# Performance work log

Measured on AMD Instinct MI355X. Metric: run time of the kernel, lower is better.

## Reference

```python
import jax, jax.numpy as jnp
import numpy as np

N, E, FEAT, C, H, D, L, T, MS, MD, NC = 20000, 320000, 128, 256, 8, 32, 5, 64, 10, 128, 2
NEG_SLOPE = 0.2


def setup_inputs() -> dict:
    key = jax.random.key(0)
    ks = jax.random.split(key, 20)
    g = lambda k, shape, fan: jax.random.normal(k, shape, jnp.float32) / np.sqrt(fan)
    return {
        "x_initial_nodes": jax.random.normal(ks[0], (N, FEAT), jnp.float32),
        "edge_index": jax.random.randint(ks[1], (2, E), 0, N, jnp.int32),
        "time_embedding": jax.random.normal(ks[2], (N, T), jnp.float32),
        "Wi": g(ks[3], (FEAT, C), FEAT),
        "bi": jnp.zeros((C,), jnp.float32),
        "Wg": g(ks[4], (L, C, C), C),          # GAT projection per layer
        "a_src": g(ks[5], (L, H, D), D),        # attention vectors
        "a_dst": g(ks[6], (L, H, D), D),
        "Wt": g(ks[7], (L, T, C), T),           # time-embedding fusion
        "Wq": g(ks[8], (L, C, C), C),           # memory cross-attention
        "Wk": g(ks[9], (L, MD, C), MD),
        "Wv": g(ks[10], (L, MD, C), MD),
        "global_memory": jax.random.normal(ks[11], (MS, MD), jnp.float32),
        "Wc": g(ks[12], (C + MD, NC), C + MD),
        "bc": jnp.zeros((NC,), jnp.float32),
    }


def _stm_layer(x, src, dst, t_proj, mem, Wg, a_s, a_d, Wq, Wk, Wv):
    # GAT-style message passing with time fusion
    h = ((x + t_proj) @ Wg).reshape(N, H, D)                      # [N,H,D]
    e_src = jnp.einsum('nhd,hd->nh', h, a_s)                      # [N,H]
    e_dst = jnp.einsum('nhd,hd->nh', h, a_d)
    logits = jax.nn.leaky_relu(e_src[src] + e_dst[dst], NEG_SLOPE)  # [E,H]
    m = jax.ops.segment_max(logits, dst, num_segments=N)
    m = jnp.where(jnp.isfinite(m), m, 0.0)                        # empty segments
    ex = jnp.exp(logits - m[dst])
    denom = jax.ops.segment_sum(ex, dst, num_segments=N)
    alpha = ex / (denom[dst] + 1e-16)                             # [E,H]
    msg = jax.ops.segment_sum(alpha[:, :, None] * h[src], dst, num_segments=N)
    node = jax.nn.relu(msg.reshape(N, C))
    # cross-attention to global memory bank
    q = node @ Wq                                                  # [N,C]
    k = mem @ Wk                                                   # [MS,C]
    v = mem @ Wv                                                   # [MS,C]
    attn = jax.nn.softmax(q @ k.T / np.sqrt(C), axis=-1)           # [N,MS]
    return jax.nn.relu(node + attn @ v + x)                        # residual


def reference(x_initial_nodes, edge_index, time_embedding, Wi, bi, Wg, a_src,
              a_dst, Wt, Wq, Wk, Wv, global_memory, Wc, bc):
    src, dst = edge_index[0], edge_index[1]
    node = jax.nn.relu(x_initial_nodes @ Wi + bi)                  # [N,C]
    for l in range(L):
        t_proj = time_embedding @ Wt[l]                            # [N,C]
        node = _stm_layer(node, src, dst, t_proj, global_memory,
                          Wg[l], a_src[l], a_dst[l], Wq[l], Wk[l], Wv[l])
    pooled = jnp.mean(node, axis=0)                                # [C]
    mem_pooled = jnp.mean(global_memory, axis=0)                   # [MD]
    final = jnp.concatenate([pooled, mem_pooled], axis=-1)         # [C+MD]
    return final @ Wc + bc                                         # [NC]
```

## Files before the change

### kernel.cpp

```cpp
#include <hip/hip_runtime.h>
#include <hip/hip_bf16.h>

#define N_NODES 20000
#define E_EDGES 320000
#define FEAT 128
#define CDIM 256
#define NHEAD 8
#define HDIM 32
#define NLAYER 5
#define TDIM 64
#define MSLOT 10
#define MDIM 128
#define NCLS 2

typedef unsigned short ushort_t;
typedef short short8 __attribute__((ext_vector_type(8)));
typedef float floatx4 __attribute__((ext_vector_type(4)));

__device__ __forceinline__ ushort_t f2bf(float f) {
    union { float f; unsigned int u; } t; t.f = f;
    unsigned int r = (t.u + 0x7FFF + ((t.u >> 16) & 1)) >> 16;
    return (ushort_t)r;
}
__device__ __forceinline__ float bf2f(ushort_t u) {
    union { float f; unsigned int u; } t; t.u = ((unsigned int)u) << 16;
    return t.f;
}

__global__ __launch_bounds__(256) void gemm_mfma(
    const ushort_t* __restrict__ A1, int lda1, int K1,
    const ushort_t* __restrict__ A2, int lda2, int Ktot,
    const ushort_t* __restrict__ Bt,
    const float* __restrict__ bias,
    float* Cf, ushort_t* Cbf, int doRelu, int M)
{
    __shared__ __align__(16) ushort_t smemA[64 * 32];
    __shared__ __align__(16) ushort_t smemB[256 * 32];
    int tid = threadIdx.x;
    int lane = tid & 63, wid = tid >> 6;
    int li = lane & 15, lq = lane >> 4;
    int row0 = blockIdx.x * 64;

    floatx4 acc[4][4];
#pragma unroll
    for (int a = 0; a < 4; a++)
#pragma unroll
        for (int b = 0; b < 4; b++) acc[a][b] = {0.f, 0.f, 0.f, 0.f};

    int ar = tid >> 2, ac = tid & 3;
    int agc = (ac - (ar >> 1)) & 3;
    int arow = row0 + ar; if (arow >= M) arow = M - 1;

    for (int k0 = 0; k0 < Ktot; k0 += 32) {
        __syncthreads();
        const ushort_t* Ab; int lda;
        if (k0 < K1) { Ab = A1 + k0; lda = lda1; }
        else         { Ab = A2 + (k0 - K1); lda = lda2; }
        {
            const void* g = (const void*)(Ab + (size_t)arow * lda + agc * 8);
            __builtin_amdgcn_global_load_lds(
                (const __attribute__((address_space(1))) void*)g,
                (__attribute__((address_space(3))) void*)&smemA[wid * 512], 16, 0, 0);
        }
#pragma unroll
        for (int j = 0; j < 4; j++) {
            int slot = wid * 256 + j * 64 + lane;
            int n = slot >> 2, c = slot & 3;
            int gc = (c - (n >> 1)) & 3;
            const void* g = (const void*)(Bt + (size_t)n * Ktot + k0 + gc * 8);
            __builtin_amdgcn_global_load_lds(
                (const __attribute__((address_space(1))) void*)g,
                (__attribute__((address_space(3))) void*)&smemB[(wid * 256 + j * 64) * 8], 16, 0, 0);
        }
        __syncthreads();

        short8 af[4], bfr[4];
#pragma unroll
        for (int mt = 0; mt < 4; mt++) {
            int m = mt * 16 + li;
            int sw = (lq + (m >> 1)) & 3;
            af[mt] = *(const short8*)&smemA[m * 32 + sw * 8];
        }
#pragma unroll
        for (int nt = 0; nt < 4; nt++) {
            int n = wid * 64 + nt * 16 + li;
            int sw = (lq + (n >> 1)) & 3;
            bfr[nt] = *(const short8*)&smemB[n * 32 + sw * 8];
        }
#pragma unroll
        for (int mt = 0; mt < 4; mt++)
#pragma unroll
            for (int nt = 0; nt < 4; nt++)
                acc[mt][nt] = __builtin_amdgcn_mfma_f32_16x16x32_bf16(af[mt], bfr[nt], acc[mt][nt], 0, 0, 0);
    }

#pragma unroll
    for (int mt = 0; mt < 4; mt++) {
        int row = row0 + mt * 16 + lq * 4;
#pragma unroll
        for (int nt = 0; nt < 4; nt++) {
            int col = wid * 64 + nt * 16 + li;
            float bv = bias ? bias[col] : 0.f;
#pragma unroll
            for (int r = 0; r < 4; r++) {
                if (row + r < M) {
                    float v = acc[mt][nt][r] + bv;
                    if (doRelu) v = fmaxf(v, 0.f);
                    if (Cf)  Cf[(size_t)(row + r) * CDIM + col] = v;
                    if (Cbf) Cbf[(size_t)(row + r) * CDIM + col] = f2bf(v);
                }
            }
        }
    }
}

__global__ __launch_bounds__(256) void gemm_h(
    const ushort_t* __restrict__ A1, int lda1, int K1,
    const ushort_t* __restrict__ A2, int lda2, int Ktot,
    const ushort_t* __restrict__ Bt,
    const float* __restrict__ a_s, const float* __restrict__ a_d,
    ushort_t* __restrict__ Cbf,
    float* __restrict__ esrc, float* __restrict__ edst, int M)
{
    __shared__ __align__(16) ushort_t smemA[64 * 32];
    __shared__ __align__(16) ushort_t smemB[256 * 32];
    __shared__ float eldsS[64][8];
    __shared__ float eldsD[64][8];
    int tid = threadIdx.x;
    int lane = tid & 63, wid = tid >> 6;
    int li = lane & 15, lq = lane >> 4;
    int row0 = blockIdx.x * 64;

    floatx4 acc[4][4];
#pragma unroll
    for (int a = 0; a < 4; a++)
#pragma unroll
        for (int b = 0; b < 4; b++) acc[a][b] = {0.f, 0.f, 0.f, 0.f};

    int ar = tid >> 2, ac = tid & 3;
    int agc = (ac - (ar >> 1)) & 3;
    int arow = row0 + ar; if (arow >= M) arow = M - 1;

    for (int k0 = 0; k0 < Ktot; k0 += 32) {
        __syncthreads();
        const ushort_t* Ab; int lda;
        if (k0 < K1) { Ab = A1 + k0; lda = lda1; }
        else         { Ab = A2 + (k0 - K1); lda = lda2; }
        {
            const void* g = (const void*)(Ab + (size_t)arow * lda + agc * 8);
            __builtin_amdgcn_global_load_lds(
                (const __attribute__((address_space(1))) void*)g,
                (__attribute__((address_space(3))) void*)&smemA[wid * 512], 16, 0, 0);
        }
#pragma unroll
        for (int j = 0; j < 4; j++) {
            int slot = wid * 256 + j * 64 + lane;
            int n = slot >> 2, c = slot & 3;
            int gc = (c - (n >> 1)) & 3;
            const void* g = (const void*)(Bt + (size_t)n * Ktot + k0 + gc * 8);
            __builtin_amdgcn_global_load_lds(
                (const __attribute__((address_space(1))) void*)g,
                (__attribute__((address_space(3))) void*)&smemB[(wid * 256 + j * 64) * 8], 16, 0, 0);
        }
        __syncthreads();

        short8 af[4], bfr[4];
#pragma unroll
        for (int mt = 0; mt < 4; mt++) {
            int m = mt * 16 + li;
            int sw = (lq + (m >> 1)) & 3;
            af[mt] = *(const short8*)&smemA[m * 32 + sw * 8];
        }
#pragma unroll
        for (int nt = 0; nt < 4; nt++) {
            int n = wid * 64 + nt * 16 + li;
            int sw = (lq + (n >> 1)) & 3;
            bfr[nt] = *(const short8*)&smemB[n * 32 + sw * 8];
        }
#pragma unroll
        for (int mt = 0; mt < 4; mt++)
#pragma unroll
            for (int nt = 0; nt < 4; nt++)
                acc[mt][nt] = __builtin_amdgcn_mfma_f32_16x16x32_bf16(af[mt], bfr[nt], acc[mt][nt], 0, 0, 0);
    }

    float as4[4], ad4[4];
#pragma unroll
    for (int nt = 0; nt < 4; nt++) {
        int col = wid * 64 + nt * 16 + li;
        as4[nt] = a_s[col];
        ad4[nt] = a_d[col];
    }
#pragma unroll
    for (int mt = 0; mt < 4; mt++) {
        int row = row0 + mt * 16 + lq * 4;
#pragma unroll
        for (int nt = 0; nt < 4; nt++) {
            int col = wid * 64 + nt * 16 + li;
#pragma unroll
            for (int r = 0; r < 4; r++)
                if (row + r < M)
                    Cbf[(size_t)(row + r) * CDIM + col] = f2bf(acc[mt][nt][r]);
        }
#pragma unroll
        for (int r = 0; r < 4; r++) {
            int row_local = mt * 16 + lq * 4 + r;
            float psA = acc[mt][0][r] * as4[0] + acc[mt][1][r] * as4[1];
            float psB = acc[mt][2][r] * as4[2] + acc[mt][3][r] * as4[3];
            float pdA = acc[mt][0][r] * ad4[0] + acc[mt][1][r] * ad4[1];
            float pdB = acc[mt][2][r] * ad4[2] + acc[mt][3][r] * ad4[3];
#pragma unroll
            for (int d = 1; d < 16; d <<= 1) {
                psA += __shfl_xor(psA, d); psB += __shfl_xor(psB, d);
                pdA += __shfl_xor(pdA, d); pdB += __shfl_xor(pdB, d);
            }
            if (li == 0) {
                eldsS[row_local][2 * wid + 0] = psA;
                eldsS[row_local][2 * wid + 1] = psB;
                eldsD[row_local][2 * wid + 0] = pdA;
                eldsD[row_local][2 * wid + 1] = pdB;
            }
        }
    }
    __syncthreads();
#pragma unroll
    for (int rr = 0; rr < 2; rr++) {
        int row = rr * 32 + (tid >> 3), hh = tid & 7;
        if (row0 + row < M) {
            esrc[(size_t)(row0 + row) * NHEAD + hh] = eldsS[row][hh];
            edst[(size_t)(row0 + row) * NHEAD + hh] = eldsD[row][hh];
        }
    }
}

__global__ __launch_bounds__(256) void gemm64(
    const float* __restrict__ A, const float* __restrict__ A2,
    const float* __restrict__ B, const float* __restrict__ bias,
    float* __restrict__ C, int M, int K, int Nf, int doRelu,
    int sA, int sB, int sC)
{
    __shared__ float As[16][64];
    __shared__ float Bs[16][64];
    A += (size_t)blockIdx.z * sA;
    B += (size_t)blockIdx.z * sB;
    C += (size_t)blockIdx.z * sC;
    int tid = threadIdx.x;
    int tx = tid & 15, ty = tid >> 4;
    int row0 = blockIdx.y * 64, col0 = blockIdx.x * 64;
    int ar = tid >> 2;
    int ac = (tid & 3) * 4;

    float acc[4][4] = {};

    for (int k0 = 0; k0 < K; k0 += 16) {
        int arow = row0 + ar;
        float4 av = make_float4(0.f, 0.f, 0.f, 0.f);
        if (arow < M) {
            av = *(const float4*)(A + (size_t)arow * K + k0 + ac);
            if (A2) {
                float4 a2 = *(const float4*)(A2 + (size_t)arow * K + k0 + ac);
                av.x += a2.x; av.y += a2.y; av.z += a2.z; av.w += a2.w;
            }
        }
        As[ac + 0][ar] = av.x;
        As[ac + 1][ar] = av.y;
        As[ac + 2][ar] = av.z;
        As[ac + 3][ar] = av.w;
        float4 bv = *(const float4*)(B + (size_t)(k0 + (tid >> 4)) * Nf + col0 + (tid & 15) * 4);
        *(float4*)&Bs[tid >> 4][(tid & 15) * 4] = bv;
        __syncthreads();
#pragma unroll
        for (int kk = 0; kk < 16; kk++) {
            float4 a = *(const float4*)&As[kk][ty * 4];
            float4 b = *(const float4*)&Bs[kk][tx * 4];
            acc[0][0] += a.x * b.x; acc[0][1] += a.x * b.y; acc[0][2] += a.x * b.z; acc[0][3] += a.x * b.w;
            acc[1][0] += a.y * b.x; acc[1][1] += a.y * b.y; acc[1][2] += a.y * b.z; acc[1][3] += a.y * b.w;
            acc[2][0] += a.z * b.x; acc[2][1] += a.z * b.y; acc[2][2] += a.z * b.z; acc[2][3] += a.z * b.w;
            acc[3][0] += a.w * b.x; acc[3][1] += a.w * b.y; acc[3][2] += a.w * b.z; acc[3][3] += a.w * b.w;
        }
        __syncthreads();
    }

    float4 bv = make_float4(0.f, 0.f, 0.f, 0.f);
    if (bias) bv = *(const float4*)(bias + col0 + tx * 4);
#pragma unroll
    for (int i = 0; i < 4; i++) {
        int r = row0 + ty * 4 + i;
        if (r < M) {
            float4 o;
            o.x = acc[i][0] + bv.x;
            o.y = acc[i][1] + bv.y;
            o.z = acc[i][2] + bv.z;
            o.w = acc[i][3] + bv.w;
            if (doRelu) {
                o.x = fmaxf(o.x, 0.f); o.y = fmaxf(o.y, 0.f);
                o.z = fmaxf(o.z, 0.f); o.w = fmaxf(o.w, 0.f);
            }
            *(float4*)(C + (size_t)r * Nf + col0 + tx * 4) = o;
        }
    }
}

__global__ void cvt_bf16(const float* __restrict__ in, ushort_t* __restrict__ out, int n)
{
    int i = blockIdx.x * blockDim.x + threadIdx.x;
    if (i < n) out[i] = f2bf(in[i]);
}

__global__ __launch_bounds__(256) void transpose_cast(
    const float* __restrict__ in, int K, int Nn,
    ushort_t* __restrict__ out, int ostride, int koff,
    int inBatchStride, int outBatchStride)
{
    __shared__ float tile[32][33];
    in  += (size_t)blockIdx.z * inBatchStride;
    out += (size_t)blockIdx.z * outBatchStride;
    int k0 = blockIdx.y * 32, n0 = blockIdx.x * 32;
    int tx = threadIdx.x & 31, ty = threadIdx.x >> 5;
#pragma unroll
    for (int j = 0; j < 4; j++)
        tile[ty + j * 8][tx] = in[(size_t)(k0 + ty + j * 8) * Nn + n0 + tx];
    __syncthreads();
#pragma unroll
    for (int j = 0; j < 4; j++) {
        int n = n0 + ty + j * 8;
        out[(size_t)n * ostride + koff + k0 + tx] = f2bf(tile[tx][ty + j * 8]);
    }
}

__global__ __launch_bounds__(256) void wqk_build(
    const float* __restrict__ Wq, const float* __restrict__ kbufs,
    float* __restrict__ wqk)
{
    int j = blockIdx.x, l = blockIdx.y;
    int d = threadIdx.x;
    __shared__ float kk[CDIM];
    kk[d] = kbufs[((size_t)l * MSLOT + j) * CDIM + d];
    __syncthreads();
    const float* wrow = Wq + ((size_t)l * CDIM + d) * CDIM;
    float acc = 0.f;
#pragma unroll 4
    for (int c = 0; c < CDIM; c++) acc += wrow[c] * kk[c];
    wqk[((size_t)l * MSLOT + j) * CDIM + d] = acc * 0.0625f;
}

__global__ void count_deg(const int* __restrict__ dst, int* __restrict__ deg, int ne)
{
    int e = blockIdx.x * blockDim.x + threadIdx.x;
    if (e < ne) atomicAdd(&deg[dst[e]], 1);
}

__global__ __launch_bounds__(1024) void scan_kernel(const int* __restrict__ deg,
                                                    int* __restrict__ offs, int n)
{
    __shared__ int swt[16];
    __shared__ int srun;
    int tid = threadIdx.x, lane = tid & 63, wid = tid >> 6;
    if (tid == 0) srun = 0;
    __syncthreads();
    for (int base = 0; base < n; base += 1024) {
        int v = (base + tid < n) ? deg[base + tid] : 0;
        int x = v;
#pragma unroll
        for (int d = 1; d < 64; d <<= 1) {
            int t = __shfl_up(x, d);
            if (lane >= d) x += t;
        }
        if (lane == 63) swt[wid] = x;
        __syncthreads();
        if (wid == 0) {
            int w = (lane < 16) ? swt[lane] : 0;
#pragma unroll
            for (int d = 1; d < 16; d <<= 1) {
                int t = __shfl_up(w, d);
                if (lane >= d) w += t;
            }
            if (lane < 16) swt[lane] = w;
        }
        __syncthreads();
        int wbase = (wid == 0) ? 0 : swt[wid - 1];
        int total = swt[15];
        int run = srun;
        if (base + tid < n) offs[base + tid] = run + wbase + x - v;
        __syncthreads();
        if (tid == 0) srun = run + total;
        __syncthreads();
    }
}

__global__ void fill_csr(const int* __restrict__ src, const int* __restrict__ dst,
                         const int* __restrict__ offs, int* __restrict__ cursor,
                         int* __restrict__ csr_src, int ne)
{
    int e = blockIdx.x * blockDim.x + threadIdx.x;
    if (e < ne) {
        int d = dst[e];
        int p = atomicAdd(&cursor[d], 1);
        csr_src[offs[d] + p] = src[e];
    }
}

__global__ __launch_bounds__(256) void gat_agg_fused(
    const ushort_t* __restrict__ h, const float* __restrict__ esrc, const float* __restrict__ edst,
    const int* __restrict__ offs, const int* __restrict__ deg, const int* __restrict__ csr_src,
    const float* __restrict__ wqk, const float* __restrict__ vbuf,
    const float* __restrict__ cur,
    float* __restrict__ outf, ushort_t* __restrict__ outbf, int n)
{
    __shared__ float alphaL[4][576];
    __shared__ int   sIdx[4][64];
    int tid = threadIdx.x;
    int lane = tid & 63;
    int wslot = tid >> 6;
    int node = blockIdx.x * 4 + wslot;
    int start = offs[node], cnt = deg[node];
    int chead = lane >> 3;

    float4 gat4;
    if (cnt <= 64) {
        int eh = lane >> 3, hh = lane & 7;
        float edl = edst[(size_t)node * NHEAD + hh];
        int sl = 0;
        if (lane < cnt) sl = csr_src[start + lane];
        sIdx[wslot][lane] = sl;
        __builtin_amdgcn_s_waitcnt(0);
        int nit = (cnt + 7) >> 3;
        float lg[8];
        float m = -3.0e38f;
        for (int it = 0; it < nit; it++) {
            int e = it * 8 + eh;
            float v = -3.0e38f;
            if (e < cnt) {
                int se = sIdx[wslot][e];
                float t = esrc[(size_t)se * NHEAD + hh] + edl;
                v = t > 0.f ? t : 0.2f * t;
            }
            lg[it] = v;
            m = fmaxf(m, v);
        }
        m = fmaxf(m, __shfl_xor(m, 8));
        m = fmaxf(m, __shfl_xor(m, 16));
        m = fmaxf(m, __shfl_xor(m, 32));
        float den = 0.f;
        for (int it = 0; it < nit; it++) {
            int e = it * 8 + eh;
            float w = 0.f;
            if (e < cnt) w = __expf(lg[it] - m);
            den += w;
            alphaL[wslot][e * 9 + hh] = w;
        }
        den += __shfl_xor(den, 8);
        den += __shfl_xor(den, 16);
        den += __shfl_xor(den, 32);
        float inv = 1.f / (den + 1e-16f);
        float invc = __shfl(inv, chead);
        __builtin_amdgcn_s_waitcnt(0);

        float4 acc = make_float4(0.f, 0.f, 0.f, 0.f);
        const float* aBase = &alphaL[wslot][chead];
        const int* sBase = sIdx[wslot];
        int rounds = (cnt + 3) >> 2;
        for (int rr = 0; rr < rounds; rr++) {
            int i0 = rr * 4;
            int s0 = sBase[i0 + 0], s1 = sBase[i0 + 1], s2 = sBase[i0 + 2], s3 = sBase[i0 + 3];
            float a0 = aBase[(i0 + 0) * 9], a1 = aBase[(i0 + 1) * 9];
            float a2 = aBase[(i0 + 2) * 9], a3 = aBase[(i0 + 3) * 9];
            ushort4 h0 = *(const ushort4*)(h + (size_t)s0 * CDIM + lane * 4);
            ushort4 h1 = *(const ushort4*)(h + (size_t)s1 * CDIM + lane * 4);
            ushort4 h2 = *(const ushort4*)(h + (size_t)s2 * CDIM + lane * 4);
            ushort4 h3 = *(const ushort4*)(h + (size_t)s3 * CDIM + lane * 4);
            acc.x += a0 * bf2f(h0.x) + a1 * bf2f(h1.x) + a2 * bf2f(h2.x) + a3 * bf2f(h3.x);
            acc.y += a0 * bf2f(h0.y) + a1 * bf2f(h1.y) + a2 * bf2f(h2.y) + a3 * bf2f(h3.y);
            acc.z += a0 * bf2f(h0.z) + a1 * bf2f(h1.z) + a2 * bf2f(h2.z) + a3 * bf2f(h3.z);
            acc.w += a0 * bf2f(h0.w) + a1 * bf2f(h1.w) + a2 * bf2f(h2.w) + a3 * bf2f(h3.w);
        }
        gat4.x = fmaxf(acc.x * invc, 0.f);
        gat4.y = fmaxf(acc.y * invc, 0.f);
        gat4.z = fmaxf(acc.z * invc, 0.f);
        gat4.w = fmaxf(acc.w * invc, 0.f);
    } else {
        int hh = lane & 7;
        float edl = edst[node * NHEAD + hh];
        float m = -3.0e38f;
        int i8 = lane >> 3;
        for (int i = 0; i < cnt; i += 8) {
            int ii = i + i8;
            if (ii < cnt) {
                int s = csr_src[start + ii];
                float lgv = esrc[s * NHEAD + hh] + edl;
                lgv = lgv > 0.f ? lgv : 0.2f * lgv;
                m = fmaxf(m, lgv);
            }
        }
        m = fmaxf(m, __shfl_xor(m, 8));
        m = fmaxf(m, __shfl_xor(m, 16));
        m = fmaxf(m, __shfl_xor(m, 32));
        float4 acc = make_float4(0.f, 0.f, 0.f, 0.f);
        float den = 0.f;
        for (int i = 0; i < cnt; i++) {
            int s = csr_src[start + i];
            float lgv = esrc[s * NHEAD + hh] + edl;
            lgv = lgv > 0.f ? lgv : 0.2f * lgv;
            float w = __expf(lgv - m);
            den += w;
            float wc = __shfl(w, chead);
            ushort4 hu = *(const ushort4*)(h + (size_t)s * CDIM + lane * 4);
            acc.x += wc * bf2f(hu.x); acc.y += wc * bf2f(hu.y);
            acc.z += wc * bf2f(hu.z); acc.w += wc * bf2f(hu.w);
        }
        float dc = __shfl(den, chead) + 1e-16f;
        float inv = 1.f / dc;
        gat4.x = fmaxf(acc.x * inv, 0.f);
        gat4.y = fmaxf(acc.y * inv, 0.f);
        gat4.z = fmaxf(acc.z * inv, 0.f);
        gat4.w = fmaxf(acc.w * inv, 0.f);
    }

    float s[MSLOT];
#pragma unroll
    for (int j = 0; j < MSLOT; j++) {
        float4 w4 = *(const float4*)(wqk + j * CDIM + lane * 4);
        s[j] = gat4.x * w4.x + gat4.y * w4.y + gat4.z * w4.z + gat4.w * w4.w;
    }
#pragma unroll
    for (int d = 1; d < 64; d <<= 1) {
#pragma unroll
        for (int j = 0; j < MSLOT; j++) s[j] += __shfl_xor(s[j], d);
    }
    float m = s[0];
#pragma unroll
    for (int j = 1; j < MSLOT; j++) m = fmaxf(m, s[j]);
    float sum = 0.f;
#pragma unroll
    for (int j = 0; j < MSLOT; j++) { s[j] = __expf(s[j] - m); sum += s[j]; }
    float inv = 1.f / sum;

    float4 c4 = *(const float4*)(cur + (size_t)node * CDIM + lane * 4);
    float4 o;
    o.x = gat4.x + c4.x; o.y = gat4.y + c4.y; o.z = gat4.z + c4.z; o.w = gat4.w + c4.w;
#pragma unroll
    for (int j = 0; j < MSLOT; j++) {
        float p = s[j] * inv;
        float4 v4 = *(const float4*)(vbuf + j * CDIM + lane * 4);
        o.x += p * v4.x; o.y += p * v4.y; o.z += p * v4.z; o.w += p * v4.w;
    }
    o.x = fmaxf(o.x, 0.f); o.y = fmaxf(o.y, 0.f); o.z = fmaxf(o.z, 0.f); o.w = fmaxf(o.w, 0.f);
    *(float4*)(outf + (size_t)node * CDIM + lane * 4) = o;
    ushort4 ob;
    ob.x = f2bf(o.x); ob.y = f2bf(o.y); ob.z = f2bf(o.z); ob.w = f2bf(o.w);
    *(ushort4*)(outbf + (size_t)node * CDIM + lane * 4) = ob;
}

__global__ void col_sum(const float* __restrict__ node, float* __restrict__ pooled, int n)
{
    float acc = 0.f;
    int c = threadIdx.x;
    for (int r = blockIdx.x; r < n; r += gridDim.x) acc += node[(size_t)r * CDIM + c];
    atomicAdd(&pooled[c], acc);
}

__global__ void finalize(const float* __restrict__ pooled, const float* __restrict__ mem,
                         const float* __restrict__ Wc, const float* __restrict__ bc,
                         float* __restrict__ out)
{
    int lane = threadIdx.x;
    float a0 = 0.f, a1 = 0.f;
    for (int i = lane; i < CDIM + MDIM; i += 64) {
        float f;
        if (i < CDIM) {
            f = pooled[i] * (1.0f / (float)N_NODES);
        } else {
            float s = 0.f;
            for (int r = 0; r < MSLOT; r++) s += mem[r * MDIM + (i - CDIM)];
            f = s * (1.0f / (float)MSLOT);
        }
        a0 += f * Wc[i * NCLS + 0];
        a1 += f * Wc[i * NCLS + 1];
    }
#pragma unroll
    for (int d = 1; d < 64; d <<= 1) { a0 += __shfl_xor(a0, d); a1 += __shfl_xor(a1, d); }
    if (lane == 0) { out[0] = a0 + bc[0]; out[1] = a1 + bc[1]; }
}

extern "C" void kernel_launch(void* const* d_in, const int* in_sizes, int n_in,
                              void* d_out, int out_size, void* d_ws, size_t ws_size,
                              hipStream_t stream)
{
    const float* x    = (const float*)d_in[0];
    const int*   ei   = (const int*)d_in[1];
    const float* temb = (const float*)d_in[2];
    const float* Wi   = (const float*)d_in[3];
    const float* bi   = (const float*)d_in[4];
    const float* Wg   = (const float*)d_in[5];
    const float* a_s  = (const float*)d_in[6];
    const float* a_d  = (const float*)d_in[7];
    const float* Wt   = (const float*)d_in[8];
    const float* Wq   = (const float*)d_in[9];
    const float* Wk   = (const float*)d_in[10];
    const float* Wv   = (const float*)d_in[11];
    const float* mem  = (const float*)d_in[12];
    const float* Wc   = (const float*)d_in[13];
    const float* bc   = (const float*)d_in[14];
    float* out = (float*)d_out;
    char* ws = (char*)d_ws;

    const size_t NC_BYTES  = (size_t)N_NODES * CDIM * 4;
    const size_t NCB_BYTES = (size_t)N_NODES * CDIM * 2;
    size_t off = 0;
    float* bufA   = (float*)(ws + off); off += NC_BYTES;
    float* bufB   = (float*)(ws + off); off += NC_BYTES;
    ushort_t* hbf    = (ushort_t*)(ws + off); off += NCB_BYTES;
    ushort_t* nodebf = (ushort_t*)(ws + off); off += NCB_BYTES;
    ushort_t* xbf    = (ushort_t*)(ws + off); off += (size_t)N_NODES * FEAT * 2;
    ushort_t* tembbf = (ushort_t*)(ws + off); off += (size_t)N_NODES * TDIM * 2;
    float* esrc   = (float*)(ws + off); off += (size_t)N_NODES * NHEAD * 4;
    float* edst   = (float*)(ws + off); off += (size_t)N_NODES * NHEAD * 4;
    float* kbufs  = (float*)(ws + off); off += (size_t)NLAYER * MSLOT * CDIM * 4;
    float* vbufs  = (float*)(ws + off); off += (size_t)NLAYER * MSLOT * CDIM * 4;
    float* wqkL   = (float*)(ws + off); off += (size_t)NLAYER * MSLOT * CDIM * 4;
    float* Wtp    = (float*)(ws + off); off += (size_t)NLAYER * TDIM * CDIM * 4;
    ushort_t* Bt_i = (ushort_t*)(ws + off); off += (size_t)CDIM * FEAT * 2;
    ushort_t* Bt_h = (ushort_t*)(ws + off); off += (size_t)NLAYER * CDIM * (CDIM + TDIM) * 2;
    size_t zero_base = off;
    float* pooled = (float*)(ws + off); off += CDIM * 4;
    int* deg      = (int*)(ws + off);   off += N_NODES * 4;
    int* cursor   = (int*)(ws + off);   off += N_NODES * 4;
    size_t zero_len = off - zero_base;
    int* offs     = (int*)(ws + off);   off += (N_NODES + 4) * 4;
    int* csr_src  = (int*)(ws + off);   off += (size_t)E_EDGES * 4;

    const int* srcIdx = ei;
    const int* dstIdx = ei + E_EDGES;

    hipMemsetAsync(ws + zero_base, 0, zero_len, stream);

    cvt_bf16<<<(N_NODES * FEAT + 255) / 256, 256, 0, stream>>>(x, xbf, N_NODES * FEAT);
    cvt_bf16<<<(N_NODES * TDIM + 255) / 256, 256, 0, stream>>>(temb, tembbf, N_NODES * TDIM);
    gemm64<<<dim3(4, 1, NLAYER), 256, 0, stream>>>(Wt, nullptr, Wg, nullptr, Wtp,
        TDIM, CDIM, CDIM, 0, TDIM * CDIM, CDIM * CDIM, TDIM * CDIM);
    transpose_cast<<<dim3(CDIM / 32, FEAT / 32, 1), 256, 0, stream>>>(
        Wi, FEAT, CDIM, Bt_i, FEAT, 0, 0, 0);
    transpose_cast<<<dim3(CDIM / 32, CDIM / 32, NLAYER), 256, 0, stream>>>(
        Wg, CDIM, CDIM, Bt_h, CDIM + TDIM, 0, CDIM * CDIM, CDIM * (CDIM + TDIM));
    transpose_cast<<<dim3(CDIM / 32, TDIM / 32, NLAYER), 256, 0, stream>>>(
        Wtp, TDIM, CDIM, Bt_h, CDIM + TDIM, CDIM, TDIM * CDIM, CDIM * (CDIM + TDIM));
    gemm64<<<dim3(4, 1, NLAYER), 256, 0, stream>>>(mem, nullptr, Wk, nullptr, kbufs,
        MSLOT, MDIM, CDIM, 0, 0, MDIM * CDIM, MSLOT * CDIM);
    gemm64<<<dim3(4, 1, NLAYER), 256, 0, stream>>>(mem, nullptr, Wv, nullptr, vbufs,
        MSLOT, MDIM, CDIM, 0, 0, MDIM * CDIM, MSLOT * CDIM);
    wqk_build<<<dim3(MSLOT, NLAYER), 256, 0, stream>>>(Wq, kbufs, wqkL);

    count_deg<<<(E_EDGES + 255) / 256, 256, 0, stream>>>(dstIdx, deg, E_EDGES);
    scan_kernel<<<1, 1024, 0, stream>>>(deg, offs, N_NODES);
    fill_csr<<<(E_EDGES + 255) / 256, 256, 0, stream>>>(srcIdx, dstIdx, offs, cursor, csr_src, E_EDGES);

    int mfmaBlocks = (N_NODES + 63) / 64;
    int nodeBlocks = N_NODES / 4;

    gemm_mfma<<<mfmaBlocks, 256, 0, stream>>>(xbf, FEAT, FEAT, nullptr, 0, FEAT,
                                              Bt_i, bi, bufA, nodebf, 1, N_NODES);

    float* cur = bufA;
    float* alt = bufB;
    for (int l = 0; l < NLAYER; l++) {
        gemm_h<<<mfmaBlocks, 256, 0, stream>>>(nodebf, CDIM, CDIM, tembbf, TDIM, CDIM + TDIM,
                                               Bt_h + (size_t)l * CDIM * (CDIM + TDIM),
                                               a_s + (size_t)l * CDIM, a_d + (size_t)l * CDIM,
                                               hbf, esrc, edst, N_NODES);
        gat_agg_fused<<<nodeBlocks, 256, 0, stream>>>(hbf, esrc, edst, offs, deg, csr_src,
                                                      wqkL + (size_t)l * MSLOT * CDIM,
                                                      vbufs + (size_t)l * MSLOT * CDIM,
                                                      cur, alt, nodebf, N_NODES);
        float* t = cur; cur = alt; alt = t;
    }

    col_sum<<<128, 256, 0, stream>>>(cur, pooled, N_NODES);
    finalize<<<1, 64, 0, stream>>>(pooled, mem, Wc, bc, out);
}
```

Before: 566.3 us.

## Split GEMM columns across blocks, register-only GAT aggregation, single-pass scan

The MFMA GEMMs now use 64x128 tiles over a 2D grid instead of 64x256 tiles. This doubles the block count for better occupancy, and attention logits are written straight from registers without an LDS stage. The GAT aggregation drops its LDS staging of indices and weights in favour of shuffles and an unrolled 8-way gather, which adds more loads in flight. The CSR scan handles all nodes in one pass, 20 per thread, instead of looping with barriers. In exchange, the A tile is loaded twice, and the unrolled gather may raise register pressure.

```diff
diff --git a/kernel.cpp b/kernel.cpp
--- a/kernel.cpp
+++ b/kernel.cpp
@@ -35,17 +35,18 @@
     float* Cf, ushort_t* Cbf, int doRelu, int M)
 {
     __shared__ __align__(16) ushort_t smemA[64 * 32];
-    __shared__ __align__(16) ushort_t smemB[256 * 32];
+    __shared__ __align__(16) ushort_t smemB[128 * 32];
     int tid = threadIdx.x;
     int lane = tid & 63, wid = tid >> 6;
     int li = lane & 15, lq = lane >> 4;
-    int row0 = blockIdx.x * 64;
-
-    floatx4 acc[4][4];
+    int row0 = blockIdx.y * 64;
+    int col0 = blockIdx.x * 128;
+
+    floatx4 acc[4][2];
 #pragma unroll
     for (int a = 0; a < 4; a++)
 #pragma unroll
-        for (int b = 0; b < 4; b++) acc[a][b] = {0.f, 0.f, 0.f, 0.f};
+        for (int b = 0; b < 2; b++) acc[a][b] = {0.f, 0.f, 0.f, 0.f};
 
     int ar = tid >> 2, ac = tid & 3;
     int agc = (ac - (ar >> 1)) & 3;
@@ -63,18 +64,18 @@
                 (__attribute__((address_space(3))) void*)&smemA[wid * 512], 16, 0, 0);
         }
 #pragma unroll
-        for (int j = 0; j < 4; j++) {
-            int slot = wid * 256 + j * 64 + lane;
+        for (int j = 0; j < 2; j++) {
+            int slot = j * 256 + tid;
             int n = slot >> 2, c = slot & 3;
             int gc = (c - (n >> 1)) & 3;
-            const void* g = (const void*)(Bt + (size_t)n * Ktot + k0 + gc * 8);
+            const void* g = (const void*)(Bt + (size_t)(col0 + n) * Ktot + k0 + gc * 8);
             __builtin_amdgcn_global_load_lds(
                 (const __attribute__((address_space(1))) void*)g,
-                (__attribute__((address_space(3))) void*)&smemB[(wid * 256 + j * 64) * 8], 16, 0, 0);
+                (__attribute__((address_space(3))) void*)&smemB[(j * 256 + wid * 64) * 8], 16, 0, 0);
         }
         __syncthreads();
 
-        short8 af[4], bfr[4];
+        short8 af[4], bfr[2];
 #pragma unroll
         for (int mt = 0; mt < 4; mt++) {
             int m = mt * 16 + li;
@@ -82,15 +83,15 @@
             af[mt] = *(const short8*)&smemA[m * 32 + sw * 8];
         }
 #pragma unroll
-        for (int nt = 0; nt < 4; nt++) {
-            int n = wid * 64 + nt * 16 + li;
-            int sw = (lq + (n >> 1)) & 3;
-            bfr[nt] = *(const short8*)&smemB[n * 32 + sw * 8];
+        for (int nt = 0; nt < 2; nt++) {
+            int nl = wid * 32 + nt * 16 + li;
+            int sw = (lq + (nl >> 1)) & 3;
+            bfr[nt] = *(const short8*)&smemB[nl * 32 + sw * 8];
         }
 #pragma unroll
         for (int mt = 0; mt < 4; mt++)
 #pragma unroll
-            for (int nt = 0; nt < 4; nt++)
+            for (int nt = 0; nt < 2; nt++)
                 acc[mt][nt] = __builtin_amdgcn_mfma_f32_16x16x32_bf16(af[mt], bfr[nt], acc[mt][nt], 0, 0, 0);
     }
 
@@ -98,8 +99,8 @@
     for (int mt = 0; mt < 4; mt++) {
         int row = row0 + mt * 16 + lq * 4;
 #pragma unroll
-        for (int nt = 0; nt < 4; nt++) {
-            int col = wid * 64 + nt * 16 + li;
+        for (int nt = 0; nt < 2; nt++) {
+            int col = col0 + wid * 32 + nt * 16 + li;
             float bv = bias ? bias[col] : 0.f;
 #pragma unroll
             for (int r = 0; r < 4; r++) {
@@ -123,19 +124,18 @@
     float* __restrict__ esrc, float* __restrict__ edst, int M)
 {
     __shared__ __align__(16) ushort_t smemA[64 * 32];
-    __shared__ __align__(16) ushort_t smemB[256 * 32];
-    __shared__ float eldsS[64][8];
-    __shared__ float eldsD[64][8];
+    __shared__ __align__(16) ushort_t smemB[128 * 32];
     int tid = threadIdx.x;
     int lane = tid & 63, wid = tid >> 6;
     int li = lane & 15, lq = lane >> 4;
-    int row0 = blockIdx.x * 64;
-
-    floatx4 acc[4][4];
+    int row0 = blockIdx.y * 64;
+    int col0 = blockIdx.x * 128;
+
+    floatx4 acc[4][2];
 #pragma unroll
     for (int a = 0; a < 4; a++)
 #pragma unroll
-        for (int b = 0; b < 4; b++) acc[a][b] = {0.f, 0.f, 0.f, 0.f};
+        for (int b = 0; b < 2; b++) acc[a][b] = {0.f, 0.f, 0.f, 0.f};
 
     int ar = tid >> 2, ac = tid & 3;
     int agc = (ac - (ar >> 1)) & 3;
@@ -153,18 +153,18 @@
                 (__attribute__((address_space(3))) void*)&smemA[wid * 512], 16, 0, 0);
         }
 #pragma unroll
-        for (int j = 0; j < 4; j++) {
-            int slot = wid * 256 + j * 64 + lane;
+        for (int j = 0; j < 2; j++) {
+            int slot = j * 256 + tid;
             int n = slot >> 2, c = slot & 3;
             int gc = (c - (n >> 1)) & 3;
-            const void* g = (const void*)(Bt + (size_t)n * Ktot + k0 + gc * 8);
+            const void* g = (const void*)(Bt + (size_t)(col0 + n) * Ktot + k0 + gc * 8);
             __builtin_amdgcn_global_load_lds(
                 (const __attribute__((address_space(1))) void*)g,
-                (__attribute__((address_space(3))) void*)&smemB[(wid * 256 + j * 64) * 8], 16, 0, 0);
+                (__attribute__((address_space(3))) void*)&smemB[(j * 256 + wid * 64) * 8], 16, 0, 0);
         }
         __syncthreads();
 
-        short8 af[4], bfr[4];
+        short8 af[4], bfr[2];
 #pragma unroll
         for (int mt = 0; mt < 4; mt++) {
             int m = mt * 16 + li;
@@ -172,31 +172,30 @@
             af[mt] = *(const short8*)&smemA[m * 32 + sw * 8];
         }
 #pragma unroll
-        for (int nt = 0; nt < 4; nt++) {
-            int n = wid * 64 + nt * 16 + li;
-            int sw = (lq + (n >> 1)) & 3;
-            bfr[nt] = *(const short8*)&smemB[n * 32 + sw * 8];
+        for (int nt = 0; nt < 2; nt++) {
+            int nl = wid * 32 + nt * 16 + li;
+            int sw = (lq + (nl >> 1)) & 3;
+            bfr[nt] = *(const short8*)&smemB[nl * 32 + sw * 8];
         }
 #pragma unroll
         for (int mt = 0; mt < 4; mt++)
 #pragma unroll
-            for (int nt = 0; nt < 4; nt++)
+            for (int nt = 0; nt < 2; nt++)
                 acc[mt][nt] = __builtin_amdgcn_mfma_f32_16x16x32_bf16(af[mt], bfr[nt], acc[mt][nt], 0, 0, 0);
     }
 
-    float as4[4], ad4[4];
-#pragma unroll
-    for (int nt = 0; nt < 4; nt++) {
-        int col = wid * 64 + nt * 16 + li;
-        as4[nt] = a_s[col];
-        ad4[nt] = a_d[col];
-    }
+    int hd = blockIdx.x * 4 + wid;
+    float as0 = a_s[col0 + wid * 32 + li];
+    float as1 = a_s[col0 + wid * 32 + 16 + li];
+    float ad0 = a_d[col0 + wid * 32 + li];
+    float ad1 = a_d[col0 + wid * 32 + 16 + li];
+
 #pragma unroll
     for (int mt = 0; mt < 4; mt++) {
         int row = row0 + mt * 16 + lq * 4;
 #pragma unroll
-        for (int nt = 0; nt < 4; nt++) {
-            int col = wid * 64 + nt * 16 + li;
+        for (int nt = 0; nt < 2; nt++) {
+            int col = col0 + wid * 32 + nt * 16 + li;
 #pragma unroll
             for (int r = 0; r < 4; r++)
                 if (row + r < M)
@@ -204,31 +203,17 @@
         }
 #pragma unroll
         for (int r = 0; r < 4; r++) {
-            int row_local = mt * 16 + lq * 4 + r;
-            float psA = acc[mt][0][r] * as4[0] + acc[mt][1][r] * as4[1];
-            float psB = acc[mt][2][r] * as4[2] + acc[mt][3][r] * as4[3];
-            float pdA = acc[mt][0][r] * ad4[0] + acc[mt][1][r] * ad4[1];
-            float pdB = acc[mt][2][r] * ad4[2] + acc[mt][3][r] * ad4[3];
+            float ps = acc[mt][0][r] * as0 + acc[mt][1][r] * as1;
+            float pd = acc[mt][0][r] * ad0 + acc[mt][1][r] * ad1;
 #pragma unroll
             for (int d = 1; d < 16; d <<= 1) {
-                psA += __shfl_xor(psA, d); psB += __shfl_xor(psB, d);
-                pdA += __shfl_xor(pdA, d); pdB += __shfl_xor(pdB, d);
-            }
-            if (li == 0) {
-                eldsS[row_local][2 * wid + 0] = psA;
-                eldsS[row_local][2 * wid + 1] = psB;
-                eldsD[row_local][2 * wid + 0] = pdA;
-                eldsD[row_local][2 * wid + 1] = pdB;
-            }
-        }
-    }
-    __syncthreads();
-#pragma unroll
-    for (int rr = 0; rr < 2; rr++) {
-        int row = rr * 32 + (tid >> 3), hh = tid & 7;
-        if (row0 + row < M) {
-            esrc[(size_t)(row0 + row) * NHEAD + hh] = eldsS[row][hh];
-            edst[(size_t)(row0 + row) * NHEAD + hh] = eldsD[row][hh];
+                ps += __shfl_xor(ps, d);
+                pd += __shfl_xor(pd, d);
+            }
+            if (li == 0 && row + r < M) {
+                esrc[(size_t)(row + r) * NHEAD + hd] = ps;
+                edst[(size_t)(row + r) * NHEAD + hd] = pd;
+            }
         }
     }
 }
@@ -354,37 +339,39 @@
                                                     int* __restrict__ offs, int n)
 {
     __shared__ int swt[16];
-    __shared__ int srun;
     int tid = threadIdx.x, lane = tid & 63, wid = tid >> 6;
-    if (tid == 0) srun = 0;
+    int base = tid * 20;
+    int v[20];
+    int s = 0;
+#pragma unroll
+    for (int i = 0; i < 20; i++) {
+        int d = (base + i < n) ? deg[base + i] : 0;
+        v[i] = d; s += d;
+    }
+    int x = s;
+#pragma unroll
+    for (int d = 1; d < 64; d <<= 1) {
+        int t = __shfl_up(x, d);
+        if (lane >= d) x += t;
+    }
+    if (lane == 63) swt[wid] = x;
     __syncthreads();
-    for (int base = 0; base < n; base += 1024) {
-        int v = (base + tid < n) ? deg[base + tid] : 0;
-        int x = v;
-#pragma unroll
-        for (int d = 1; d < 64; d <<= 1) {
-            int t = __shfl_up(x, d);
-            if (lane >= d) x += t;
-        }
-        if (lane == 63) swt[wid] = x;
-        __syncthreads();
-        if (wid == 0) {
-            int w = (lane < 16) ? swt[lane] : 0;
-#pragma unroll
-            for (int d = 1; d < 16; d <<= 1) {
-                int t = __shfl_up(w, d);
-                if (lane >= d) w += t;
-            }
-            if (lane < 16) swt[lane] = w;
-        }
-        __syncthreads();
-        int wbase = (wid == 0) ? 0 : swt[wid - 1];
-        int total = swt[15];
-        int run = srun;
-        if (base + tid < n) offs[base + tid] = run + wbase + x - v;
-        __syncthreads();
-        if (tid == 0) srun = run + total;
-        __syncthreads();
+    if (wid == 0) {
+        int w = (lane < 16) ? swt[lane] : 0;
+#pragma unroll
+        for (int d = 1; d < 16; d <<= 1) {
+            int t = __shfl_up(w, d);
+            if (lane >= d) w += t;
+        }
+        if (lane < 16) swt[lane] = w;
+    }
+    __syncthreads();
+    int wbase = (wid == 0) ? 0 : swt[wid - 1];
+    int run = wbase + x - s;
+#pragma unroll
+    for (int i = 0; i < 20; i++) {
+        if (base + i < n) offs[base + i] = run;
+        run += v[i];
     }
 }
 
@@ -407,8 +394,6 @@
     const float* __restrict__ cur,
     float* __restrict__ outf, ushort_t* __restrict__ outbf, int n)
 {
-    __shared__ float alphaL[4][576];
-    __shared__ int   sIdx[4][64];
     int tid = threadIdx.x;
     int lane = tid & 63;
     int wslot = tid >> 6;
@@ -420,20 +405,20 @@
     if (cnt <= 64) {
         int eh = lane >> 3, hh = lane & 7;
         float edl = edst[(size_t)node * NHEAD + hh];
-        int sl = 0;
-        if (lane < cnt) sl = csr_src[start + lane];
-        sIdx[wslot][lane] = sl;
-        __builtin_amdgcn_s_waitcnt(0);
+        int sl = (lane < cnt) ? csr_src[start + lane] : 0;
         int nit = (cnt + 7) >> 3;
-        float lg[8];
+        float lg[8], w8[8];
         float m = -3.0e38f;
-        for (int it = 0; it < nit; it++) {
-            int e = it * 8 + eh;
+#pragma unroll
+        for (int it = 0; it < 8; it++) {
             float v = -3.0e38f;
-            if (e < cnt) {
-                int se = sIdx[wslot][e];
-                float t = esrc[(size_t)se * NHEAD + hh] + edl;
-                v = t > 0.f ? t : 0.2f * t;
+            if (it < nit) {
+                int e = it * 8 + eh;
+                int se = __shfl(sl, e);
+                if (e < cnt) {
+                    float t = esrc[(size_t)se * NHEAD + hh] + edl;
+                    v = t > 0.f ? t : 0.2f * t;
+                }
             }
             lg[it] = v;
             m = fmaxf(m, v);
@@ -442,37 +427,44 @@
         m = fmaxf(m, __shfl_xor(m, 16));
         m = fmaxf(m, __shfl_xor(m, 32));
         float den = 0.f;
-        for (int it = 0; it < nit; it++) {
-            int e = it * 8 + eh;
+#pragma unroll
+        for (int it = 0; it < 8; it++) {
             float w = 0.f;
-            if (e < cnt) w = __expf(lg[it] - m);
+            if (it < nit) {
+                int e = it * 8 + eh;
+                if (e < cnt) w = __expf(lg[it] - m);
+            }
+            w8[it] = w;
             den += w;
-            alphaL[wslot][e * 9 + hh] = w;
         }
         den += __shfl_xor(den, 8);
         den += __shfl_xor(den, 16);
         den += __shfl_xor(den, 32);
         float inv = 1.f / (den + 1e-16f);
         float invc = __shfl(inv, chead);
-        __builtin_amdgcn_s_waitcnt(0);
 
         float4 acc = make_float4(0.f, 0.f, 0.f, 0.f);
-        const float* aBase = &alphaL[wslot][chead];
-        const int* sBase = sIdx[wslot];
-        int rounds = (cnt + 3) >> 2;
-        for (int rr = 0; rr < rounds; rr++) {
-            int i0 = rr * 4;
-            int s0 = sBase[i0 + 0], s1 = sBase[i0 + 1], s2 = sBase[i0 + 2], s3 = sBase[i0 + 3];
-            float a0 = aBase[(i0 + 0) * 9], a1 = aBase[(i0 + 1) * 9];
-            float a2 = aBase[(i0 + 2) * 9], a3 = aBase[(i0 + 3) * 9];
-            ushort4 h0 = *(const ushort4*)(h + (size_t)s0 * CDIM + lane * 4);
-            ushort4 h1 = *(const ushort4*)(h + (size_t)s1 * CDIM + lane * 4);
-            ushort4 h2 = *(const ushort4*)(h + (size_t)s2 * CDIM + lane * 4);
-            ushort4 h3 = *(const ushort4*)(h + (size_t)s3 * CDIM + lane * 4);
-            acc.x += a0 * bf2f(h0.x) + a1 * bf2f(h1.x) + a2 * bf2f(h2.x) + a3 * bf2f(h3.x);
-            acc.y += a0 * bf2f(h0.y) + a1 * bf2f(h1.y) + a2 * bf2f(h2.y) + a3 * bf2f(h3.y);
-            acc.z += a0 * bf2f(h0.z) + a1 * bf2f(h1.z) + a2 * bf2f(h2.z) + a3 * bf2f(h3.z);
-            acc.w += a0 * bf2f(h0.w) + a1 * bf2f(h1.w) + a2 * bf2f(h2.w) + a3 * bf2f(h3.w);
+#pragma unroll
+        for (int rr = 0; rr < 8; rr++) {
+            if (rr < nit) {
+                int sv[8]; float av[8];
+#pragma unroll
+                for (int k = 0; k < 8; k++) {
+                    sv[k] = __shfl(sl, rr * 8 + k);
+                    av[k] = __shfl(w8[rr], (k << 3) | chead);
+                }
+                ushort4 hv[8];
+#pragma unroll
+                for (int k = 0; k < 8; k++)
+                    hv[k] = *(const ushort4*)(h + (size_t)sv[k] * CDIM + lane * 4);
+#pragma unroll
+                for (int k = 0; k < 8; k++) {
+                    acc.x += av[k] * bf2f(hv[k].x);
+                    acc.y += av[k] * bf2f(hv[k].y);
+                    acc.z += av[k] * bf2f(hv[k].z);
+                    acc.w += av[k] * bf2f(hv[k].w);
+                }
+            }
         }
         gat4.x = fmaxf(acc.x * invc, 0.f);
         gat4.y = fmaxf(acc.y * invc, 0.f);
@@ -480,14 +472,14 @@
         gat4.w = fmaxf(acc.w * invc, 0.f);
     } else {
         int hh = lane & 7;
-        float edl = edst[node * NHEAD + hh];
+        float edl = edst[(size_t)node * NHEAD + hh];
         float m = -3.0e38f;
         int i8 = lane >> 3;
         for (int i = 0; i < cnt; i += 8) {
             int ii = i + i8;
             if (ii < cnt) {
                 int s = csr_src[start + ii];
-                float lgv = esrc[s * NHEAD + hh] + edl;
+                float lgv = esrc[(size_t)s * NHEAD + hh] + edl;
                 lgv = lgv > 0.f ? lgv : 0.2f * lgv;
                 m = fmaxf(m, lgv);
             }
@@ -499,7 +491,7 @@
         float den = 0.f;
         for (int i = 0; i < cnt; i++) {
             int s = csr_src[start + i];
-            float lgv = esrc[s * NHEAD + hh] + edl;
+            float lgv = esrc[(size_t)s * NHEAD + hh] + edl;
             lgv = lgv > 0.f ? lgv : 0.2f * lgv;
             float w = __expf(lgv - m);
             den += w;
@@ -654,19 +646,19 @@
     scan_kernel<<<1, 1024, 0, stream>>>(deg, offs, N_NODES);
     fill_csr<<<(E_EDGES + 255) / 256, 256, 0, stream>>>(srcIdx, dstIdx, offs, cursor, csr_src, E_EDGES);
 
-    int mfmaBlocks = (N_NODES + 63) / 64;
+    dim3 mfmaGrid(2, (N_NODES + 63) / 64);
     int nodeBlocks = N_NODES / 4;
 
-    gemm_mfma<<<mfmaBlocks, 256, 0, stream>>>(xbf, FEAT, FEAT, nullptr, 0, FEAT,
-                                              Bt_i, bi, bufA, nodebf, 1, N_NODES);
+    gemm_mfma<<<mfmaGrid, 256, 0, stream>>>(xbf, FEAT, FEAT, nullptr, 0, FEAT,
+                                            Bt_i, bi, bufA, nodebf, 1, N_NODES);
 
     float* cur = bufA;
     float* alt = bufB;
     for (int l = 0; l < NLAYER; l++) {
-        gemm_h<<<mfmaBlocks, 256, 0, stream>>>(nodebf, CDIM, CDIM, tembbf, TDIM, CDIM + TDIM,
-                                               Bt_h + (size_t)l * CDIM * (CDIM + TDIM),
-                                               a_s + (size_t)l * CDIM, a_d + (size_t)l * CDIM,
-                                               hbf, esrc, edst, N_NODES);
+        gemm_h<<<mfmaGrid, 256, 0, stream>>>(nodebf, CDIM, CDIM, tembbf, TDIM, CDIM + TDIM,
+                                             Bt_h + (size_t)l * CDIM * (CDIM + TDIM),
+                                             a_s + (size_t)l * CDIM, a_d + (size_t)l * CDIM,
+                                             hbf, esrc, edst, N_NODES);
         gat_agg_fused<<<nodeBlocks, 256, 0, stream>>>(hbf, esrc, edst, offs, deg, csr_src,
                                                       wqkL + (size_t)l * MSLOT * CDIM,
                                                       vbufs + (size_t)l * MSLOT * CDIM,
```

Result: faster. 518.0 us (-8.5%).
